# Kernel tuning notes

Hardware: AMD Instinct MI355X
Metric: run time of the kernel (lower is better)

## Reference

```python
import jax, jax.numpy as jnp
import numpy as np

# HT config: input_shape = output_shape = (8,8,8,8), rank = 8, d = 4 modes
B = 4096
M = 8      # per-mode input dim
N = 8      # per-mode output dim
R = 8      # HT rank
FEAT = M ** 4  # 4096


def setup_inputs() -> dict:
    key = jax.random.key(0)
    ks = jax.random.split(key, 8)
    x = jax.random.normal(ks[0], (B, FEAT), dtype=jnp.float32)
    # leaf factors: (in_p, out_p, rank); xavier-style scale over the input mode
    f_std = np.float32(np.sqrt(2.0 / (M + N * R)))
    F0 = jax.random.normal(ks[1], (M, N, R), dtype=jnp.float32) * f_std
    F1 = jax.random.normal(ks[2], (M, N, R), dtype=jnp.float32) * f_std
    F2 = jax.random.normal(ks[3], (M, N, R), dtype=jnp.float32) * f_std
    F3 = jax.random.normal(ks[4], (M, N, R), dtype=jnp.float32) * f_std
    # internal cores: (left_rank, right_rank, parent_rank)
    c_std = np.float32(np.sqrt(2.0 / (R + R * R)))
    CL = jax.random.normal(ks[5], (R, R, R), dtype=jnp.float32) * c_std
    CR = jax.random.normal(ks[6], (R, R, R), dtype=jnp.float32) * c_std
    bound = np.float32(1.0 / np.sqrt(FEAT))
    bias = jax.random.uniform(ks[7], (FEAT,), dtype=jnp.float32, minval=-bound, maxval=bound)
    return {"x": x, "F0": F0, "F1": F1, "F2": F2, "F3": F3,
            "CL": CL, "CR": CR, "bias": bias}


def reference(x, F0, F1, F2, F3, CL, CR, bias):
    b = x.shape[0]
    # (b, i, j, k, l): one axis per HT mode
    x4 = x.reshape(b, M, M, M, M)
    # Pre-contract each subtree's two leaves with its core (tiny tensors):
    # left transfer  W_L[i, j, a, c, p], right transfer W_R[k, l, d, e, p].
    # This is the same tensor-network contraction as the tn.Node graph,
    # just in an efficient associativity order.
    WL = jnp.einsum('iar,jcs,rsp->ijacp', F0, F1, CL)
    WR = jnp.einsum('kdr,les,rsp->kldep', F2, F3, CR)
    # contract left subtree against the input: (b, k, l, a, c, p)
    yL = jnp.einsum('bijkl,ijacp->bklacp', x4, WL)
    # contract right subtree; parent edges of the two subtrees are joined (p)
    y = jnp.einsum('bklacp,kldep->bacde', yL, WR)
    return y.reshape(b, FEAT) + bias
```

## Files before the change

### kernel.cpp

```cpp
#include <hip/hip_runtime.h>


typedef short bf16x8 __attribute__((ext_vector_type(8)));
typedef float f32x4  __attribute__((ext_vector_type(4)));

static __device__ __forceinline__ unsigned short f2bf(float f) {
    unsigned int u = __float_as_uint(f);
    u = (u + 0x7FFFu + ((u >> 16) & 1u)) >> 16;
    return (unsigned short)u;
}

__global__ void ht_precompute(const float* __restrict__ F0, const float* __restrict__ F1,
                              const float* __restrict__ F2, const float* __restrict__ F3,
                              const float* __restrict__ CL, const float* __restrict__ CR,
                              unsigned short* __restrict__ frags) {
    int idx = blockIdx.x * blockDim.x + threadIdx.x;
    int isW = idx >> 15;
    int r15 = idx & 32767;
    int p    = r15 >> 12;
    int f    = (r15 >> 9) & 7;
    int lane = (r15 >> 3) & 63;
    int j    = r15 & 7;
    int cb = f >> 1, ks = f & 1;
    int n = cb * 16 + (lane & 15);
    int k = ks * 32 + ((lane >> 4) & 3) * 8 + j;
    const float* Fa = isW ? F2 : F0;
    const float* Fb = isW ? F3 : F1;
    const float* C  = isW ? CR : CL;
    int i1 = k >> 3, i2 = k & 7, o1 = n >> 3, o2 = n & 7;
    float acc = 0.f;
    for (int r = 0; r < 8; ++r) {
        float fa = Fa[(i1 * 8 + o1) * 8 + r];
        for (int s = 0; s < 8; ++s)
            acc += fa * Fb[(i2 * 8 + o2) * 8 + s] * C[(r * 8 + s) * 8 + p];
    }
    frags[(size_t)isW * 32768 + ((p * 8 + f) << 9) + lane * 8 + j] = f2bf(acc);
}

__global__ __launch_bounds__(64) void ht_main(const float* __restrict__ x,
                                              const unsigned short* __restrict__ frags,
                                              const float* __restrict__ bias,
                                              float* __restrict__ out) {
    __shared__ unsigned short Tl[64 * 72];
    const int b    = blockIdx.x;
    const int lane = threadIdx.x;
    const int l15  = lane & 15;
    const int q    = lane >> 4;

    bf16x8 xf[4][2];
    const float* xb = x + ((size_t)b << 12);
#pragma unroll
    for (int rb = 0; rb < 4; ++rb)
#pragma unroll
        for (int ks = 0; ks < 2; ++ks) {
            const float* src = xb + (ks * 32 + q * 8) * 64 + rb * 16 + l15;
#pragma unroll
            for (int j = 0; j < 8; ++j)
                xf[rb][ks][j] = (short)f2bf(src[j * 64]);
        }

    f32x4 acc[4][4];
#pragma unroll
    for (int i = 0; i < 4; ++i)
#pragma unroll
        for (int j = 0; j < 4; ++j)
            acc[i][j] = f32x4{0.f, 0.f, 0.f, 0.f};

    const unsigned short* AF = frags;
    const unsigned short* WF = frags + 32768;

#pragma unroll 1
    for (int p = 0; p < 8; ++p) {
        bf16x8 af[4][2];
#pragma unroll
        for (int cb = 0; cb < 4; ++cb)
#pragma unroll
            for (int ks = 0; ks < 2; ++ks)
                af[cb][ks] = *(const bf16x8*)(AF + (((p * 8 + cb * 2 + ks) << 9) + lane * 8));
#pragma unroll
        for (int rb = 0; rb < 4; ++rb) {
#pragma unroll
            for (int cb = 0; cb < 4; ++cb) {
                f32x4 t = f32x4{0.f, 0.f, 0.f, 0.f};
                t = __builtin_amdgcn_mfma_f32_16x16x32_bf16(xf[rb][0], af[cb][0], t, 0, 0, 0);
                t = __builtin_amdgcn_mfma_f32_16x16x32_bf16(xf[rb][1], af[cb][1], t, 0, 0, 0);
                int ac = cb * 16 + l15;
                int kl = rb * 16 + q * 4;
                ushort4 w;
                w.x = f2bf(t[0]); w.y = f2bf(t[1]); w.z = f2bf(t[2]); w.w = f2bf(t[3]);
                *(ushort4*)(&Tl[ac * 72 + kl]) = w;
            }
        }
        bf16x8 wf[4][2];
#pragma unroll
        for (int cb = 0; cb < 4; ++cb)
#pragma unroll
            for (int ks = 0; ks < 2; ++ks)
                wf[cb][ks] = *(const bf16x8*)(WF + (((p * 8 + cb * 2 + ks) << 9) + lane * 8));
        bf16x8 tf[4][2];
#pragma unroll
        for (int rb = 0; rb < 4; ++rb)
#pragma unroll
            for (int ks = 0; ks < 2; ++ks) {
                int ac = rb * 16 + l15;
                int kl = ks * 32 + q * 8;
                tf[rb][ks] = *(const bf16x8*)(&Tl[ac * 72 + kl]);
            }
#pragma unroll
        for (int rb = 0; rb < 4; ++rb)
#pragma unroll
            for (int cb = 0; cb < 4; ++cb) {
                acc[rb][cb] = __builtin_amdgcn_mfma_f32_16x16x32_bf16(tf[rb][0], wf[cb][0], acc[rb][cb], 0, 0, 0);
                acc[rb][cb] = __builtin_amdgcn_mfma_f32_16x16x32_bf16(tf[rb][1], wf[cb][1], acc[rb][cb], 0, 0, 0);
            }
    }

    float* ob = out + ((size_t)b << 12);
#pragma unroll
    for (int rb = 0; rb < 4; ++rb)
#pragma unroll
        for (int cb = 0; cb < 4; ++cb) {
            int de  = cb * 16 + l15;
            int ac0 = rb * 16 + q * 4;
#pragma unroll
            for (int r = 0; r < 4; ++r) {
                int o = (ac0 + r) * 64 + de;
                ob[o] = acc[rb][cb][r] + bias[o];
            }
        }
}

extern "C" void kernel_launch(void* const* d_in, const int* in_sizes, int n_in,
                              void* d_out, int out_size, void* d_ws, size_t ws_size,
                              hipStream_t stream) {
    const float* x    = (const float*)d_in[0];
    const float* F0   = (const float*)d_in[1];
    const float* F1   = (const float*)d_in[2];
    const float* F2   = (const float*)d_in[3];
    const float* F3   = (const float*)d_in[4];
    const float* CL   = (const float*)d_in[5];
    const float* CR   = (const float*)d_in[6];
    const float* bias = (const float*)d_in[7];
    float* out = (float*)d_out;
    unsigned short* frags = (unsigned short*)d_ws;

    const int B = in_sizes[0] / 4096;

    ht_precompute<<<256, 256, 0, stream>>>(F0, F1, F2, F3, CL, CR, frags);
    ht_main<<<B, 64, 0, stream>>>(x, frags, bias, out);
}
```

Before: 153.8 us.

## Pack four samples per block, use hardware bf16 pair conversion, repitch LDS

Each block now runs four independent wavefronts, one per batch row, each with its own LDS slice, instead of one 64-thread block per row. The aim is to cut per-block launch and scheduling overhead and give the CU more resident waves. Float-to-bf16 conversion now goes through the packed __float22bfloat162_rn intrinsic rather than manual bit rounding. The LDS row pitch changes from 72 to 68 to reduce bank conflicts, so the 16-byte fragment reads are split into two 8-byte reads for alignment. The launch grid now assumes the batch size is divisible by 4.

After: 150.0 us. 2.5% less time.

```diff
diff --git a/kernel.cpp b/kernel.cpp
--- a/kernel.cpp
+++ b/kernel.cpp
@@ -1,8 +1,20 @@
 #include <hip/hip_runtime.h>
+#include <hip/hip_bf16.h>
 
 
 typedef short bf16x8 __attribute__((ext_vector_type(8)));
 typedef float f32x4  __attribute__((ext_vector_type(4)));
+
+union Frag8 {
+    bf16x8 v;
+    unsigned int u4[4];
+    uint2 u2[2];
+};
+
+static __device__ __forceinline__ unsigned int pkbf(float a, float b) {
+    __hip_bfloat162 h = __float22bfloat162_rn(float2{a, b});
+    return *reinterpret_cast<unsigned int*>(&h);
+}
 
 static __device__ __forceinline__ unsigned short f2bf(float f) {
     unsigned int u = __float_as_uint(f);
@@ -37,17 +49,23 @@
     frags[(size_t)isW * 32768 + ((p * 8 + f) << 9) + lane * 8 + j] = f2bf(acc);
 }
 
-__global__ __launch_bounds__(64) void ht_main(const float* __restrict__ x,
-                                              const unsigned short* __restrict__ frags,
-                                              const float* __restrict__ bias,
-                                              float* __restrict__ out) {
-    __shared__ unsigned short Tl[64 * 72];
-    const int b    = blockIdx.x;
-    const int lane = threadIdx.x;
-    const int l15  = lane & 15;
-    const int q    = lane >> 4;
+#define T_PITCH 68
 
-    bf16x8 xf[4][2];
+__global__ __launch_bounds__(256) void ht_main(const float* __restrict__ x,
+                                               const unsigned short* __restrict__ frags,
+                                               const float* __restrict__ bias,
+                                               float* __restrict__ out) {
+    __shared__ unsigned short Tl[4 * 64 * T_PITCH];
+    const int tid  = threadIdx.x;
+    const int lane = tid & 63;
+    const int w    = __builtin_amdgcn_readfirstlane(tid >> 6);
+    const int b    = blockIdx.x * 4 + w;
+    unsigned short* Tw = Tl + w * (64 * T_PITCH);
+
+    const int l15 = lane & 15;
+    const int q   = lane >> 4;
+
+    Frag8 xf[4][2];
     const float* xb = x + ((size_t)b << 12);
 #pragma unroll
     for (int rb = 0; rb < 4; ++rb)
@@ -55,8 +73,8 @@
         for (int ks = 0; ks < 2; ++ks) {
             const float* src = xb + (ks * 32 + q * 8) * 64 + rb * 16 + l15;
 #pragma unroll
-            for (int j = 0; j < 8; ++j)
-                xf[rb][ks][j] = (short)f2bf(src[j * 64]);
+            for (int j = 0; j < 8; j += 2)
+                xf[rb][ks].u4[j >> 1] = pkbf(src[j * 64], src[(j + 1) * 64]);
         }
 
     f32x4 acc[4][4];
@@ -71,47 +89,49 @@
 
 #pragma unroll 1
     for (int p = 0; p < 8; ++p) {
-        bf16x8 af[4][2];
+        Frag8 af[4][2];
 #pragma unroll
         for (int cb = 0; cb < 4; ++cb)
 #pragma unroll
             for (int ks = 0; ks < 2; ++ks)
-                af[cb][ks] = *(const bf16x8*)(AF + (((p * 8 + cb * 2 + ks) << 9) + lane * 8));
+                af[cb][ks].v = *(const bf16x8*)(AF + (((p * 8 + cb * 2 + ks) << 9) + lane * 8));
 #pragma unroll
         for (int rb = 0; rb < 4; ++rb) {
 #pragma unroll
             for (int cb = 0; cb < 4; ++cb) {
                 f32x4 t = f32x4{0.f, 0.f, 0.f, 0.f};
-                t = __builtin_amdgcn_mfma_f32_16x16x32_bf16(xf[rb][0], af[cb][0], t, 0, 0, 0);
-                t = __builtin_amdgcn_mfma_f32_16x16x32_bf16(xf[rb][1], af[cb][1], t, 0, 0, 0);
+                t = __builtin_amdgcn_mfma_f32_16x16x32_bf16(xf[rb][0].v, af[cb][0].v, t, 0, 0, 0);
+                t = __builtin_amdgcn_mfma_f32_16x16x32_bf16(xf[rb][1].v, af[cb][1].v, t, 0, 0, 0);
                 int ac = cb * 16 + l15;
                 int kl = rb * 16 + q * 4;
-                ushort4 w;
-                w.x = f2bf(t[0]); w.y = f2bf(t[1]); w.z = f2bf(t[2]); w.w = f2bf(t[3]);
-                *(ushort4*)(&Tl[ac * 72 + kl]) = w;
+                uint2 wv;
+                wv.x = pkbf(t[0], t[1]);
+                wv.y = pkbf(t[2], t[3]);
+                *(uint2*)(&Tw[ac * T_PITCH + kl]) = wv;
             }
         }
-        bf16x8 wf[4][2];
+        Frag8 wf[4][2];
 #pragma unroll
         for (int cb = 0; cb < 4; ++cb)
 #pragma unroll
             for (int ks = 0; ks < 2; ++ks)
-                wf[cb][ks] = *(const bf16x8*)(WF + (((p * 8 + cb * 2 + ks) << 9) + lane * 8));
-        bf16x8 tf[4][2];
+                wf[cb][ks].v = *(const bf16x8*)(WF + (((p * 8 + cb * 2 + ks) << 9) + lane * 8));
+        Frag8 tf[4][2];
 #pragma unroll
         for (int rb = 0; rb < 4; ++rb)
 #pragma unroll
             for (int ks = 0; ks < 2; ++ks) {
                 int ac = rb * 16 + l15;
                 int kl = ks * 32 + q * 8;
-                tf[rb][ks] = *(const bf16x8*)(&Tl[ac * 72 + kl]);
+                tf[rb][ks].u2[0] = *(const uint2*)(&Tw[ac * T_PITCH + kl]);
+                tf[rb][ks].u2[1] = *(const uint2*)(&Tw[ac * T_PITCH + kl + 4]);
             }
 #pragma unroll
         for (int rb = 0; rb < 4; ++rb)
 #pragma unroll
             for (int cb = 0; cb < 4; ++cb) {
-                acc[rb][cb] = __builtin_amdgcn_mfma_f32_16x16x32_bf16(tf[rb][0], wf[cb][0], acc[rb][cb], 0, 0, 0);
-                acc[rb][cb] = __builtin_amdgcn_mfma_f32_16x16x32_bf16(tf[rb][1], wf[cb][1], acc[rb][cb], 0, 0, 0);
+                acc[rb][cb] = __builtin_amdgcn_mfma_f32_16x16x32_bf16(tf[rb][0].v, wf[cb][0].v, acc[rb][cb], 0, 0, 0);
+                acc[rb][cb] = __builtin_amdgcn_mfma_f32_16x16x32_bf16(tf[rb][1].v, wf[cb][1].v, acc[rb][cb], 0, 0, 0);
             }
     }
 
@@ -147,5 +167,5 @@
     const int B = in_sizes[0] / 4096;
 
     ht_precompute<<<256, 256, 0, stream>>>(F0, F1, F2, F3, CL, CR, frags);
-    ht_main<<<B, 64, 0, stream>>>(x, frags, bias, out);
+    ht_main<<<B / 4, 256, 0, stream>>>(x, frags, bias, out);
 }
```
